# Optimization experiments

Hardware: AMD Instinct MI355X
Metric: run time of the kernel (lower is better)

The kernel has to match this reference:

```python
import jax, jax.numpy as jnp
import numpy as np

D_MODEL = 1024
N_HEADS = 16
D_K = D_MODEL // N_HEADS


def setup_inputs() -> dict:
    key = jax.random.key(0)
    ks = jax.random.split(key, 11)
    B, S = 4, 2048
    scale = 1.0 / np.sqrt(D_MODEL)
    inp = {
        "Q": jax.random.normal(ks[0], (B, S, D_MODEL), jnp.float32),
        "K": jax.random.normal(ks[1], (B, S, D_MODEL), jnp.float32),
        "V": jax.random.normal(ks[2], (B, S, D_MODEL), jnp.float32),
        "Wq": jax.random.normal(ks[3], (D_MODEL, D_MODEL), jnp.float32) * scale,
        "bq": jnp.zeros((D_MODEL,), jnp.float32),
        "Wk": jax.random.normal(ks[4], (D_MODEL, D_MODEL), jnp.float32) * scale,
        "bk": jnp.zeros((D_MODEL,), jnp.float32),
        "Wv": jax.random.normal(ks[5], (D_MODEL, D_MODEL), jnp.float32) * scale,
        "bv": jnp.zeros((D_MODEL,), jnp.float32),
        "Wo": jax.random.normal(ks[6], (D_MODEL, D_MODEL), jnp.float32) * scale,
        "bo": jnp.zeros((D_MODEL,), jnp.float32),
    }
    return inp


def _split_heads(x):
    B, S, _ = x.shape
    return x.reshape(B, S, N_HEADS, D_K).transpose(0, 2, 1, 3)  # [B,H,S,Dk]


def reference(Q, K, V, Wq, bq, Wk, bk, Wv, bv, Wo, bo):
    # torch nn.Linear: y = x @ W.T + b
    q = _split_heads(Q @ Wq.T + bq)
    k = _split_heads(K @ Wk.T + bk)
    v = _split_heads(V @ Wv.T + bv)
    scores = jnp.einsum("bhsd,bhtd->bhst", q, k) / jnp.sqrt(jnp.float32(D_K))
    probs = jax.nn.softmax(scores, axis=-1)
    attn = jnp.einsum("bhst,bhtd->bhsd", probs, v)  # [B,H,S,Dk]
    B, H, S, Dk = attn.shape
    combined = attn.transpose(0, 2, 1, 3).reshape(B, S, H * Dk)
    return combined @ Wo.T + bo
```

## Files before the change

### kernel.cpp

```cpp
#include <hip/hip_runtime.h>
#include <hip/hip_bf16.h>

typedef float  f32x4  __attribute__((ext_vector_type(4)));
typedef float  f32x16 __attribute__((ext_vector_type(16)));
typedef float  fvec4  __attribute__((ext_vector_type(4)));
typedef __bf16 bf16x8 __attribute__((ext_vector_type(8)));
typedef unsigned short u16x4 __attribute__((ext_vector_type(4)));
typedef unsigned short u16x8 __attribute__((ext_vector_type(8)));
typedef unsigned int   u32x4 __attribute__((ext_vector_type(4)));

#define DEVINL __device__ __forceinline__

constexpr int D_MODEL = 1024;
constexpr int NH      = 16;
constexpr int DK      = 64;
constexpr int SEQ     = 2048;
constexpr int BATCH   = 4;
constexpr int M_TOK   = BATCH * SEQ;

DEVINL unsigned short f32_to_bf16_u(float f) {
    unsigned int u = __builtin_bit_cast(unsigned int, f);
    u = (u + 0x7FFFu + ((u >> 16) & 1u)) >> 16;
    return (unsigned short)u;
}

DEVINL float exp2_fast(float x) { return __builtin_amdgcn_exp2f(x); }

DEVINL unsigned cvt_pk_bf16(float lo, float hi_) {
    unsigned d;
    asm("v_cvt_pk_bf16_f32 %0, %1, %2" : "=v"(d) : "v"(lo), "v"(hi_));
    return d;
}

DEVINL void gload_lds16(const void* g, void* l) {
    __builtin_amdgcn_global_load_lds(
        (const __attribute__((address_space(1))) void*)g,
        (__attribute__((address_space(3))) void*)l, 16, 0, 0);
}

__global__ __launch_bounds__(256) void cvt4(const float* __restrict__ a,
                                            const float* __restrict__ b,
                                            const float* __restrict__ c,
                                            const float* __restrict__ d,
                                            unsigned short* __restrict__ dst, int n8)
{
    int y = blockIdx.y;
    const float* s = (y == 0) ? a : (y == 1) ? b : (y == 2) ? c : d;
    size_t i = blockIdx.x * 256 + threadIdx.x;
    fvec4 v0 = *reinterpret_cast<const fvec4*>(s + i * 8);
    fvec4 v1 = *reinterpret_cast<const fvec4*>(s + i * 8 + 4);
    bf16x8 o;
    #pragma unroll
    for (int j = 0; j < 4; ++j) { o[j] = (__bf16)v0[j]; o[j + 4] = (__bf16)v1[j]; }
    *reinterpret_cast<bf16x8*>(dst + ((size_t)y * n8 + i) * 8) = o;
}

__global__ __launch_bounds__(256) void cvt3(const float* __restrict__ a,
                                            const float* __restrict__ b,
                                            const float* __restrict__ c,
                                            unsigned short* __restrict__ dst, int n8)
{
    int y = blockIdx.y;
    const float* s = (y == 0) ? a : (y == 1) ? b : c;
    size_t i = blockIdx.x * 256 + threadIdx.x;
    fvec4 v0 = *reinterpret_cast<const fvec4*>(s + i * 8);
    fvec4 v1 = *reinterpret_cast<const fvec4*>(s + i * 8 + 4);
    bf16x8 o;
    #pragma unroll
    for (int j = 0; j < 4; ++j) { o[j] = (__bf16)v0[j]; o[j + 4] = (__bf16)v1[j]; }
    *reinterpret_cast<bf16x8*>(dst + ((size_t)y * n8 + i) * 8) = o;
}

template<bool A_BF16, int OMODE>
__global__ __launch_bounds__(256) void gemm_nt(const void* __restrict__ Ap,
                                               const unsigned short* __restrict__ Wb,
                                               const float* __restrict__ bias,
                                               void* __restrict__ outp,
                                               float out_scale)
{
    constexpr int K = D_MODEL, N = D_MODEL;
    __shared__ char As_[128 * 64 * 2];
    __shared__ char Bs_[128 * 64 * 2];

    const int tid  = threadIdx.x;
    const int lane = tid & 63;
    const int wave = tid >> 6;
    const int wr = (wave >> 1) * 64;
    const int wc = (wave & 1) * 64;
    const int wg = ((int)blockIdx.x & 7) * 64 + ((int)blockIdx.x >> 3);
    const int n0 = (wg & 7) * 128;
    const int m0 = (wg >> 3) * 128;
    const int l15 = lane & 15, h16 = lane >> 4;

    f32x4 acc[4][4] = {};

    for (int kt = 0; kt < K; kt += 64) {
        __syncthreads();
        #pragma unroll
        for (int i = 0; i < 4; ++i) {
            int chunk = tid + i * 256;
            int r = chunk >> 3, c16 = chunk & 7;
            int cs = (c16 ^ (r & 7)) * 8;
            gload_lds16(Wb + (size_t)(n0 + r) * K + kt + cs, Bs_ + chunk * 16);
            if constexpr (A_BF16) {
                gload_lds16((const unsigned short*)Ap + (size_t)(m0 + r) * K + kt + cs,
                            As_ + chunk * 16);
            } else {
                const float* src = (const float*)Ap + (size_t)(m0 + r) * K + kt + c16 * 8;
                fvec4 v0 = *reinterpret_cast<const fvec4*>(src);
                fvec4 v1 = *reinterpret_cast<const fvec4*>(src + 4);
                bf16x8 o;
                #pragma unroll
                for (int j = 0; j < 4; ++j) { o[j] = (__bf16)v0[j]; o[j + 4] = (__bf16)v1[j]; }
                *reinterpret_cast<bf16x8*>(As_ + ((chunk * 16) ^ ((r & 7) << 4))) = o;
            }
        }
        __syncthreads();

        #pragma unroll
        for (int kk = 0; kk < 2; ++kk) {
            bf16x8 af[4], bfr[4];
            #pragma unroll
            for (int mi = 0; mi < 4; ++mi) {
                int r = wr + mi * 16 + l15;
                af[mi] = *reinterpret_cast<const bf16x8*>(
                    As_ + ((r * 128 + kk * 64 + h16 * 16) ^ ((r & 7) << 4)));
            }
            #pragma unroll
            for (int ni = 0; ni < 4; ++ni) {
                int r = wc + ni * 16 + l15;
                bfr[ni] = *reinterpret_cast<const bf16x8*>(
                    Bs_ + ((r * 128 + kk * 64 + h16 * 16) ^ ((r & 7) << 4)));
            }
            #pragma unroll
            for (int mi = 0; mi < 4; ++mi)
                #pragma unroll
                for (int ni = 0; ni < 4; ++ni)
                    acc[mi][ni] = __builtin_amdgcn_mfma_f32_16x16x32_bf16(
                        af[mi], bfr[ni], acc[mi][ni], 0, 0, 0);
        }
    }

    const int rl = h16 * 4;
    #pragma unroll
    for (int mi = 0; mi < 4; ++mi) {
        #pragma unroll
        for (int ni = 0; ni < 4; ++ni) {
            int col = n0 + wc + ni * 16 + l15;
            float bv = bias[col];
            if constexpr (OMODE == 2) {
                int row0 = m0 + wr + mi * 16 + rl;
                int bb = row0 >> 11, s0 = row0 & (SEQ - 1);
                int h = col >> 6, dk = col & (DK - 1);
                u16x4 o;
                #pragma unroll
                for (int r = 0; r < 4; ++r)
                    o[r] = f32_to_bf16_u((acc[mi][ni][r] + bv) * out_scale);
                *reinterpret_cast<u16x4*>((unsigned short*)outp +
                    (((size_t)bb * NH + h) * DK + dk) * SEQ + s0) = o;
            } else {
                #pragma unroll
                for (int r = 0; r < 4; ++r) {
                    int row = m0 + wr + mi * 16 + rl + r;
                    float v = (acc[mi][ni][r] + bv) * out_scale;
                    if constexpr (OMODE == 1) {
                        int bb = row >> 11, s = row & (SEQ - 1);
                        int h = col >> 6, dk = col & (DK - 1);
                        ((unsigned short*)outp)[((((size_t)bb * NH + h) * SEQ) + s) * DK + dk]
                            = f32_to_bf16_u(v);
                    } else {
                        ((float*)outp)[(size_t)row * N + col] = v;
                    }
                }
            }
        }
    }
}

__global__ __launch_bounds__(512, 4) void attn_kernel(const unsigned short* __restrict__ qb,
                                                      const unsigned short* __restrict__ kb,
                                                      const unsigned short* __restrict__ vt,
                                                      unsigned short* __restrict__ ob)
{
    constexpr float THR = 11.0f;
    __shared__ char lds[32768];

    const int tid  = threadIdx.x;
    const int lane = tid & 63;
    const int tl31 = lane & 31;
    const int hi   = lane >> 5;
    const int wave = tid >> 6;
    const int wg   = ((int)blockIdx.x & 7) * 64 + ((int)blockIdx.x >> 3);
    const int bh   = wg >> 3;
    const int q0   = (wg & 7) * 256;
    const size_t base  = (size_t)bh * SEQ * DK;
    const size_t baseT = (size_t)bh * DK * SEQ;

    const int k_kt = tid >> 8, k_kd = (tid >> 6) & 3, k_hi = (tid >> 5) & 1, k_tl = tid & 31;
    const size_t k_goff = base + (size_t)(k_kt * 32 + k_tl) * DK + k_kd * 16 + k_hi * 8;
    const int v_tg = tid >> 6, v_dh = (tid >> 5) & 1, v_dl = tid & 31;
    const size_t v_goff = baseT + (size_t)(v_dh * 32 + v_dl) * SEQ + v_tg * 8;

    bf16x8 qf[4];
    #pragma unroll
    for (int kd = 0; kd < 4; ++kd)
        qf[kd] = *reinterpret_cast<const bf16x8*>(
            qb + base + (size_t)(q0 + wave * 32 + tl31) * DK + kd * 16 + hi * 8);

    f32x16 oaccT[2] = {};
    float m_run = -1e30f, l_run = 0.f;

    {
        u16x8 kreg = *reinterpret_cast<const u16x8*>(kb + k_goff);
        u16x8 vreg = *reinterpret_cast<const u16x8*>(vt + v_goff);
        *reinterpret_cast<u16x8*>(lds + tid * 16) = kreg;
        *reinterpret_cast<u16x8*>(lds + 8192 + tid * 16) = vreg;
    }
    __syncthreads();

    for (int t = 0; t < 32; ++t) {
        const int cur = t & 1;
        const char* Kr = lds + cur * 16384;
        const char* Vr = Kr + 8192;

        u16x8 kreg, vreg;
        if (t < 31) {
            const int t0n = (t + 1) * 64;
            kreg = *reinterpret_cast<const u16x8*>(kb + k_goff + (size_t)t0n * DK);
            vreg = *reinterpret_cast<const u16x8*>(vt + v_goff + t0n);
        }

        f32x16 sT[2] = {};
        #pragma unroll
        for (int kt = 0; kt < 2; ++kt)
            #pragma unroll
            for (int kd = 0; kd < 4; ++kd) {
                bf16x8 kf = *reinterpret_cast<const bf16x8*>(Kr + kt * 4096 + kd * 1024 + lane * 16);
                sT[kt] = __builtin_amdgcn_mfma_f32_32x32x16_bf16(kf, qf[kd], sT[kt], 0, 0, 0);
            }

        float m = sT[0][0];
        #pragma unroll
        for (int kt = 0; kt < 2; ++kt)
            #pragma unroll
            for (int i = 0; i < 16; ++i) m = fmaxf(m, sT[kt][i]);
        m = fmaxf(m, __shfl_xor(m, 32));
        if (__any(m > m_run + THR)) {
            float mn = fmaxf(m_run, m);
            float al = exp2_fast(m_run - mn);
            m_run = mn;
            l_run *= al;
            oaccT[0] *= al;
            oaccT[1] *= al;
        }
        {
            float rs0 = 0.f, rs1 = 0.f, rs2 = 0.f, rs3 = 0.f;
            #pragma unroll
            for (int kt = 0; kt < 2; ++kt)
                #pragma unroll
                for (int i = 0; i < 16; i += 4) {
                    float p0 = exp2_fast(sT[kt][i + 0] - m_run);
                    float p1 = exp2_fast(sT[kt][i + 1] - m_run);
                    float p2 = exp2_fast(sT[kt][i + 2] - m_run);
                    float p3 = exp2_fast(sT[kt][i + 3] - m_run);
                    sT[kt][i + 0] = p0; sT[kt][i + 1] = p1;
                    sT[kt][i + 2] = p2; sT[kt][i + 3] = p3;
                    rs0 += p0; rs1 += p1; rs2 += p2; rs3 += p3;
                }
            float rs = (rs0 + rs1) + (rs2 + rs3);
            rs += __shfl_xor(rs, 32);
            l_run += rs;
        }

        #pragma unroll
        for (int ks = 0; ks < 4; ++ks) {
            bf16x8 vfA0 = *reinterpret_cast<const bf16x8*>(Vr + ks * 2048 + hi * 1024 + tl31 * 16);
            bf16x8 vfA1 = *reinterpret_cast<const bf16x8*>(Vr + ks * 2048 + hi * 1024 + 512 + tl31 * 16);
            const int kt = ks >> 1, b = (ks & 1) * 8;
            unsigned a0 = cvt_pk_bf16(sT[kt][b + 0], sT[kt][b + 1]);
            unsigned a1 = cvt_pk_bf16(sT[kt][b + 2], sT[kt][b + 3]);
            unsigned a2 = cvt_pk_bf16(sT[kt][b + 4], sT[kt][b + 5]);
            unsigned a3 = cvt_pk_bf16(sT[kt][b + 6], sT[kt][b + 7]);
            unsigned z0 = __shfl_xor(hi ? a0 : a2, 32);
            unsigned z1 = __shfl_xor(hi ? a1 : a3, 32);
            u32x4 w;
            w[0] = hi ? z0 : a0;
            w[1] = hi ? z1 : a1;
            w[2] = hi ? a2 : z0;
            w[3] = hi ? a3 : z1;
            bf16x8 pa = __builtin_bit_cast(bf16x8, w);
            oaccT[0] = __builtin_amdgcn_mfma_f32_32x32x16_bf16(vfA0, pa, oaccT[0], 0, 0, 0);
            oaccT[1] = __builtin_amdgcn_mfma_f32_32x32x16_bf16(vfA1, pa, oaccT[1], 0, 0, 0);
        }

        if (t < 31) {
            char* Kw = lds + (cur ^ 1) * 16384;
            *reinterpret_cast<u16x8*>(Kw + tid * 16) = kreg;
            *reinterpret_cast<u16x8*>(Kw + 8192 + tid * 16) = vreg;
        }
        __syncthreads();
    }

    char* myregion = lds + wave * 4096;
    const int bb = bh >> 4, h = bh & 15;
    {
        float rl = 1.0f / l_run;
        #pragma unroll
        for (int dh = 0; dh < 2; ++dh)
            #pragma unroll
            for (int r = 0; r < 16; ++r) {
                int dl = (r & 3) + 8 * (r >> 2) + 4 * hi + 32 * dh;
                int boff = (tl31 * 128 + dl * 2) ^ ((tl31 & 7) << 4);
                *reinterpret_cast<unsigned short*>(myregion + boff) =
                    f32_to_bf16_u(oaccT[dh][r] * rl);
            }
        #pragma unroll
        for (int c = 0; c < 4; ++c) {
            int chunk = lane + c * 64;
            int row = chunk >> 3, c16 = chunk & 7;
            int boff = (row * 128 + c16 * 16) ^ ((row & 7) << 4);
            u16x8 v = *reinterpret_cast<const u16x8*>(myregion + boff);
            size_t tok = (size_t)(bb * SEQ) + q0 + wave * 32 + row;
            *reinterpret_cast<u16x8*>(ob + tok * D_MODEL + h * DK + c16 * 8) = v;
        }
    }
}

extern "C" void kernel_launch(void* const* d_in, const int* in_sizes, int n_in,
                              void* d_out, int out_size, void* d_ws, size_t ws_size,
                              hipStream_t stream)
{
    const float* Q  = (const float*)d_in[0];
    const float* K_ = (const float*)d_in[1];
    const float* V  = (const float*)d_in[2];
    const float* Wq = (const float*)d_in[3];
    const float* bq = (const float*)d_in[4];
    const float* Wk = (const float*)d_in[5];
    const float* bk = (const float*)d_in[6];
    const float* Wv = (const float*)d_in[7];
    const float* bv = (const float*)d_in[8];
    const float* Wo = (const float*)d_in[9];
    const float* bo = (const float*)d_in[10];
    float* out = (float*)d_out;

    const size_t SZ = (size_t)M_TOK * D_MODEL;
    const size_t WZ = (size_t)D_MODEL * D_MODEL;
    unsigned short* qh_ = (unsigned short*)d_ws;
    unsigned short* kh_ = qh_ + SZ;
    unsigned short* vh_ = kh_ + SZ;
    unsigned short* ah_ = vh_ + SZ;
    unsigned short* wqb = ah_ + SZ;
    unsigned short* wkb = wqb + WZ;
    unsigned short* wvb = wkb + WZ;
    unsigned short* wob = wvb + WZ;
    unsigned short* qbf = wob + WZ;
    unsigned short* kbf = qbf + SZ;
    unsigned short* vbf = kbf + SZ;

    const bool big = ws_size >= (size_t)(4 * SZ + 4 * WZ + 3 * SZ) * 2;
    const float qscale = 0.125f * 1.4426950408889634f;

    cvt4<<<dim3((int)(WZ / 8 / 256), 4), 256, 0, stream>>>(Wq, Wk, Wv, Wo, wqb, (int)(WZ / 8));

    if (big) {
        cvt3<<<dim3((int)(SZ / 8 / 256), 3), 256, 0, stream>>>(Q, K_, V, qbf, (int)(SZ / 8));
        gemm_nt<true, 1><<<512, 256, 0, stream>>>(qbf, wqb, bq, qh_, qscale);
        gemm_nt<true, 1><<<512, 256, 0, stream>>>(kbf, wkb, bk, kh_, 1.0f);
        gemm_nt<true, 2><<<512, 256, 0, stream>>>(vbf, wvb, bv, vh_, 1.0f);
    } else {
        gemm_nt<false, 1><<<512, 256, 0, stream>>>(Q,  wqb, bq, qh_, qscale);
        gemm_nt<false, 1><<<512, 256, 0, stream>>>(K_, wkb, bk, kh_, 1.0f);
        gemm_nt<false, 2><<<512, 256, 0, stream>>>(V,  wvb, bv, vh_, 1.0f);
    }
    attn_kernel<<<512, 512, 0, stream>>>(qh_, kh_, vh_, ah_);
    gemm_nt<true, 0><<<512, 256, 0, stream>>>(ah_, wob, bo, out, 1.0f);
}
```

Before: 217.8 us.

## Merge QKV projections into one launch and pre-permute V to drop P shuffles

```diff
diff --git a/kernel.cpp b/kernel.cpp
--- a/kernel.cpp
+++ b/kernel.cpp
@@ -25,6 +25,7 @@
 }
 
 DEVINL float exp2_fast(float x) { return __builtin_amdgcn_exp2f(x); }
+DEVINL float mx3(float a, float b, float c) { return fmaxf(fmaxf(a, b), c); }
 
 DEVINL unsigned cvt_pk_bf16(float lo, float hi_) {
     unsigned d;
@@ -37,6 +38,8 @@
         (const __attribute__((address_space(1))) void*)g,
         (__attribute__((address_space(3))) void*)l, 16, 0, 0);
 }
+
+DEVINL int vperm_s(int s0) { return (s0 & ~12) | ((s0 & 4) << 1) | ((s0 & 8) >> 1); }
 
 __global__ __launch_bounds__(256) void cvt4(const float* __restrict__ a,
                                             const float* __restrict__ b,
@@ -71,16 +74,24 @@
     *reinterpret_cast<bf16x8*>(dst + ((size_t)y * n8 + i) * 8) = o;
 }
 
-template<bool A_BF16, int OMODE>
-__global__ __launch_bounds__(256) void gemm_nt(const void* __restrict__ Ap,
-                                               const unsigned short* __restrict__ Wb,
-                                               const float* __restrict__ bias,
-                                               void* __restrict__ outp,
-                                               float out_scale)
+template<bool QKV>
+__global__ __launch_bounds__(256) void gemm_bf(
+    const unsigned short* __restrict__ A0, const unsigned short* __restrict__ W0,
+    const float* __restrict__ B0, void* __restrict__ O0,
+    const unsigned short* __restrict__ A1, const unsigned short* __restrict__ W1,
+    const float* __restrict__ B1, void* __restrict__ O1,
+    const unsigned short* __restrict__ A2, const unsigned short* __restrict__ W2,
+    const float* __restrict__ B2, void* __restrict__ O2,
+    float qscale)
 {
     constexpr int K = D_MODEL, N = D_MODEL;
     __shared__ char As_[128 * 64 * 2];
     __shared__ char Bs_[128 * 64 * 2];
+
+    const int y = QKV ? (int)blockIdx.y : 0;
+    const unsigned short* Ap = (y == 0) ? A0 : (y == 1) ? A1 : A2;
+    const unsigned short* Wb = (y == 0) ? W0 : (y == 1) ? W1 : W2;
+    const float* bias = (y == 0) ? B0 : (y == 1) ? B1 : B2;
 
     const int tid  = threadIdx.x;
     const int lane = tid & 63;
@@ -102,18 +113,114 @@
             int r = chunk >> 3, c16 = chunk & 7;
             int cs = (c16 ^ (r & 7)) * 8;
             gload_lds16(Wb + (size_t)(n0 + r) * K + kt + cs, Bs_ + chunk * 16);
-            if constexpr (A_BF16) {
-                gload_lds16((const unsigned short*)Ap + (size_t)(m0 + r) * K + kt + cs,
-                            As_ + chunk * 16);
+            gload_lds16(Ap + (size_t)(m0 + r) * K + kt + cs, As_ + chunk * 16);
+        }
+        __syncthreads();
+
+        #pragma unroll
+        for (int kk = 0; kk < 2; ++kk) {
+            bf16x8 af[4], bfr[4];
+            #pragma unroll
+            for (int mi = 0; mi < 4; ++mi) {
+                int r = wr + mi * 16 + l15;
+                af[mi] = *reinterpret_cast<const bf16x8*>(
+                    As_ + ((r * 128 + kk * 64 + h16 * 16) ^ ((r & 7) << 4)));
+            }
+            #pragma unroll
+            for (int ni = 0; ni < 4; ++ni) {
+                int r = wc + ni * 16 + l15;
+                bfr[ni] = *reinterpret_cast<const bf16x8*>(
+                    Bs_ + ((r * 128 + kk * 64 + h16 * 16) ^ ((r & 7) << 4)));
+            }
+            #pragma unroll
+            for (int mi = 0; mi < 4; ++mi)
+                #pragma unroll
+                for (int ni = 0; ni < 4; ++ni)
+                    acc[mi][ni] = __builtin_amdgcn_mfma_f32_16x16x32_bf16(
+                        af[mi], bfr[ni], acc[mi][ni], 0, 0, 0);
+        }
+    }
+
+    const int rl = h16 * 4;
+    #pragma unroll
+    for (int mi = 0; mi < 4; ++mi) {
+        #pragma unroll
+        for (int ni = 0; ni < 4; ++ni) {
+            int col = n0 + wc + ni * 16 + l15;
+            float bv = bias[col];
+            if constexpr (QKV) {
+                float sc = (y == 0) ? qscale : 1.0f;
+                if (y == 2) {
+                    int row0 = m0 + wr + mi * 16 + rl;
+                    int bb = row0 >> 11, s0 = row0 & (SEQ - 1);
+                    int sp = vperm_s(s0);
+                    int h = col >> 6, dk = col & (DK - 1);
+                    u16x4 o;
+                    #pragma unroll
+                    for (int r = 0; r < 4; ++r)
+                        o[r] = f32_to_bf16_u(acc[mi][ni][r] + bv);
+                    *reinterpret_cast<u16x4*>((unsigned short*)O2 +
+                        (((size_t)bb * NH + h) * DK + dk) * SEQ + sp) = o;
+                } else {
+                    unsigned short* op = (unsigned short*)((y == 0) ? O0 : O1);
+                    #pragma unroll
+                    for (int r = 0; r < 4; ++r) {
+                        int row = m0 + wr + mi * 16 + rl + r;
+                        int bb = row >> 11, s = row & (SEQ - 1);
+                        int h = col >> 6, dk = col & (DK - 1);
+                        op[((((size_t)bb * NH + h) * SEQ) + s) * DK + dk]
+                            = f32_to_bf16_u((acc[mi][ni][r] + bv) * sc);
+                    }
+                }
             } else {
-                const float* src = (const float*)Ap + (size_t)(m0 + r) * K + kt + c16 * 8;
-                fvec4 v0 = *reinterpret_cast<const fvec4*>(src);
-                fvec4 v1 = *reinterpret_cast<const fvec4*>(src + 4);
-                bf16x8 o;
-                #pragma unroll
-                for (int j = 0; j < 4; ++j) { o[j] = (__bf16)v0[j]; o[j + 4] = (__bf16)v1[j]; }
-                *reinterpret_cast<bf16x8*>(As_ + ((chunk * 16) ^ ((r & 7) << 4))) = o;
-            }
+                #pragma unroll
+                for (int r = 0; r < 4; ++r) {
+                    int row = m0 + wr + mi * 16 + rl + r;
+                    ((float*)O0)[(size_t)row * N + col] = acc[mi][ni][r] + bv;
+                }
+            }
+        }
+    }
+}
+
+template<int OMODE>
+__global__ __launch_bounds__(256) void gemm_f32a(const float* __restrict__ Ap,
+                                                 const unsigned short* __restrict__ Wb,
+                                                 const float* __restrict__ bias,
+                                                 void* __restrict__ outp,
+                                                 float out_scale)
+{
+    constexpr int K = D_MODEL, N = D_MODEL;
+    __shared__ char As_[128 * 64 * 2];
+    __shared__ char Bs_[128 * 64 * 2];
+
+    const int tid  = threadIdx.x;
+    const int lane = tid & 63;
+    const int wave = tid >> 6;
+    const int wr = (wave >> 1) * 64;
+    const int wc = (wave & 1) * 64;
+    const int wg = ((int)blockIdx.x & 7) * 64 + ((int)blockIdx.x >> 3);
+    const int n0 = (wg & 7) * 128;
+    const int m0 = (wg >> 3) * 128;
+    const int l15 = lane & 15, h16 = lane >> 4;
+
+    f32x4 acc[4][4] = {};
+
+    for (int kt = 0; kt < K; kt += 64) {
+        __syncthreads();
+        #pragma unroll
+        for (int i = 0; i < 4; ++i) {
+            int chunk = tid + i * 256;
+            int r = chunk >> 3, c16 = chunk & 7;
+            int cs = (c16 ^ (r & 7)) * 8;
+            gload_lds16(Wb + (size_t)(n0 + r) * K + kt + cs, Bs_ + chunk * 16);
+            const float* src = Ap + (size_t)(m0 + r) * K + kt + c16 * 8;
+            fvec4 v0 = *reinterpret_cast<const fvec4*>(src);
+            fvec4 v1 = *reinterpret_cast<const fvec4*>(src + 4);
+            bf16x8 o;
+            #pragma unroll
+            for (int j = 0; j < 4; ++j) { o[j] = (__bf16)v0[j]; o[j + 4] = (__bf16)v1[j]; }
+            *reinterpret_cast<bf16x8*>(As_ + ((chunk * 16) ^ ((r & 7) << 4))) = o;
         }
         __syncthreads();
 
@@ -151,26 +258,22 @@
             if constexpr (OMODE == 2) {
                 int row0 = m0 + wr + mi * 16 + rl;
                 int bb = row0 >> 11, s0 = row0 & (SEQ - 1);
+                int sp = vperm_s(s0);
                 int h = col >> 6, dk = col & (DK - 1);
                 u16x4 o;
                 #pragma unroll
                 for (int r = 0; r < 4; ++r)
                     o[r] = f32_to_bf16_u((acc[mi][ni][r] + bv) * out_scale);
                 *reinterpret_cast<u16x4*>((unsigned short*)outp +
-                    (((size_t)bb * NH + h) * DK + dk) * SEQ + s0) = o;
+                    (((size_t)bb * NH + h) * DK + dk) * SEQ + sp) = o;
             } else {
                 #pragma unroll
                 for (int r = 0; r < 4; ++r) {
                     int row = m0 + wr + mi * 16 + rl + r;
-                    float v = (acc[mi][ni][r] + bv) * out_scale;
-                    if constexpr (OMODE == 1) {
-                        int bb = row >> 11, s = row & (SEQ - 1);
-                        int h = col >> 6, dk = col & (DK - 1);
-                        ((unsigned short*)outp)[((((size_t)bb * NH + h) * SEQ) + s) * DK + dk]
-                            = f32_to_bf16_u(v);
-                    } else {
-                        ((float*)outp)[(size_t)row * N + col] = v;
-                    }
+                    int bb = row >> 11, s = row & (SEQ - 1);
+                    int h = col >> 6, dk = col & (DK - 1);
+                    ((unsigned short*)outp)[((((size_t)bb * NH + h) * SEQ) + s) * DK + dk]
+                        = f32_to_bf16_u((acc[mi][ni][r] + bv) * out_scale);
                 }
             }
         }
@@ -239,12 +342,21 @@
                 sT[kt] = __builtin_amdgcn_mfma_f32_32x32x16_bf16(kf, qf[kd], sT[kt], 0, 0, 0);
             }
 
-        float m = sT[0][0];
-        #pragma unroll
-        for (int kt = 0; kt < 2; ++kt)
-            #pragma unroll
-            for (int i = 0; i < 16; ++i) m = fmaxf(m, sT[kt][i]);
-        m = fmaxf(m, __shfl_xor(m, 32));
+        float m;
+        {
+            float tm[2];
+            #pragma unroll
+            for (int kt = 0; kt < 2; ++kt) {
+                float g0 = mx3(sT[kt][0],  sT[kt][1],  sT[kt][2]);
+                float g1 = mx3(sT[kt][3],  sT[kt][4],  sT[kt][5]);
+                float g2 = mx3(sT[kt][6],  sT[kt][7],  sT[kt][8]);
+                float g3 = mx3(sT[kt][9],  sT[kt][10], sT[kt][11]);
+                float g4 = mx3(sT[kt][12], sT[kt][13], sT[kt][14]);
+                tm[kt] = fmaxf(mx3(g0, g1, g2), mx3(g3, g4, sT[kt][15]));
+            }
+            m = fmaxf(tm[0], tm[1]);
+            m = fmaxf(m, __shfl_xor(m, 32));
+        }
         if (__any(m > m_run + THR)) {
             float mn = fmaxf(m_run, m);
             float al = exp2_fast(m_run - mn);
@@ -276,18 +388,12 @@
         for (int ks = 0; ks < 4; ++ks) {
             bf16x8 vfA0 = *reinterpret_cast<const bf16x8*>(Vr + ks * 2048 + hi * 1024 + tl31 * 16);
             bf16x8 vfA1 = *reinterpret_cast<const bf16x8*>(Vr + ks * 2048 + hi * 1024 + 512 + tl31 * 16);
-            const int kt = ks >> 1, b = (ks & 1) * 8;
-            unsigned a0 = cvt_pk_bf16(sT[kt][b + 0], sT[kt][b + 1]);
-            unsigned a1 = cvt_pk_bf16(sT[kt][b + 2], sT[kt][b + 3]);
-            unsigned a2 = cvt_pk_bf16(sT[kt][b + 4], sT[kt][b + 5]);
-            unsigned a3 = cvt_pk_bf16(sT[kt][b + 6], sT[kt][b + 7]);
-            unsigned z0 = __shfl_xor(hi ? a0 : a2, 32);
-            unsigned z1 = __shfl_xor(hi ? a1 : a3, 32);
+            const int kt = ks >> 1, r0 = (ks & 1) * 8;
             u32x4 w;
-            w[0] = hi ? z0 : a0;
-            w[1] = hi ? z1 : a1;
-            w[2] = hi ? a2 : z0;
-            w[3] = hi ? a3 : z1;
+            w[0] = cvt_pk_bf16(sT[kt][r0 + 0], sT[kt][r0 + 1]);
+            w[1] = cvt_pk_bf16(sT[kt][r0 + 2], sT[kt][r0 + 3]);
+            w[2] = cvt_pk_bf16(sT[kt][r0 + 4], sT[kt][r0 + 5]);
+            w[3] = cvt_pk_bf16(sT[kt][r0 + 6], sT[kt][r0 + 7]);
             bf16x8 pa = __builtin_bit_cast(bf16x8, w);
             oaccT[0] = __builtin_amdgcn_mfma_f32_32x32x16_bf16(vfA0, pa, oaccT[0], 0, 0, 0);
             oaccT[1] = __builtin_amdgcn_mfma_f32_32x32x16_bf16(vfA1, pa, oaccT[1], 0, 0, 0);
@@ -364,14 +470,15 @@
 
     if (big) {
         cvt3<<<dim3((int)(SZ / 8 / 256), 3), 256, 0, stream>>>(Q, K_, V, qbf, (int)(SZ / 8));
-        gemm_nt<true, 1><<<512, 256, 0, stream>>>(qbf, wqb, bq, qh_, qscale);
-        gemm_nt<true, 1><<<512, 256, 0, stream>>>(kbf, wkb, bk, kh_, 1.0f);
-        gemm_nt<true, 2><<<512, 256, 0, stream>>>(vbf, wvb, bv, vh_, 1.0f);
+        gemm_bf<true><<<dim3(512, 3), 256, 0, stream>>>(
+            qbf, wqb, bq, qh_,  kbf, wkb, bk, kh_,  vbf, wvb, bv, vh_, qscale);
     } else {
-        gemm_nt<false, 1><<<512, 256, 0, stream>>>(Q,  wqb, bq, qh_, qscale);
-        gemm_nt<false, 1><<<512, 256, 0, stream>>>(K_, wkb, bk, kh_, 1.0f);
-        gemm_nt<false, 2><<<512, 256, 0, stream>>>(V,  wvb, bv, vh_, 1.0f);
+        gemm_f32a<1><<<512, 256, 0, stream>>>(Q,  wqb, bq, qh_, qscale);
+        gemm_f32a<1><<<512, 256, 0, stream>>>(K_, wkb, bk, kh_, 1.0f);
+        gemm_f32a<2><<<512, 256, 0, stream>>>(V,  wvb, bv, vh_, 1.0f);
     }
     attn_kernel<<<512, 512, 0, stream>>>(qh_, kh_, vh_, ah_);
-    gemm_nt<true, 0><<<512, 256, 0, stream>>>(ah_, wob, bo, out, 1.0f);
-}
+    gemm_bf<false><<<dim3(512, 1), 256, 0, stream>>>(
+        ah_, wob, bo, out,  nullptr, nullptr, nullptr, nullptr,
+        nullptr, nullptr, nullptr, nullptr, 1.0f);
+}
```

New measurement: 203.7 us. 1.07x faster.
